# Optimization experiments

Measured on AMD Instinct MI355X. Metric: run time of the kernel, lower is better.

## Reference

```python
import jax, jax.numpy as jnp
import numpy as np

D = 1024          # n_embd
H = 4 * D         # SwiGLU hidden
E = 8             # num_experts
K = 2             # top_k
B, T = 2, 2048

def setup_inputs() -> dict:
    key = jax.random.key(0)
    ks = jax.random.split(key, 12)
    s = 0.02
    return {
        "x":   jax.random.normal(ks[0], (B, T, D), jnp.float32),
        "noise": jax.random.normal(ks[1], (B, T, E), jnp.float32),
        # router (nn.Linear with bias=True by default)
        "Wr": jax.random.normal(ks[2], (D, E), jnp.float32) * s,
        "br": jnp.zeros((E,), jnp.float32),
        "Wn": jax.random.normal(ks[3], (D, E), jnp.float32) * s,
        "bn": jnp.zeros((E,), jnp.float32),
        # routed experts, stacked over E (bias=False)
        "Wg": jax.random.normal(ks[4], (E, D, H), jnp.float32) * s,
        "Wu": jax.random.normal(ks[5], (E, D, H), jnp.float32) * s,
        "Wd": jax.random.normal(ks[6], (E, H, D), jnp.float32) * s,
        # shared expert (num_shared_experts = 1)
        "Sg": jax.random.normal(ks[7], (D, H), jnp.float32) * s,
        "Su": jax.random.normal(ks[8], (D, H), jnp.float32) * s,
        "Sd": jax.random.normal(ks[9], (H, D), jnp.float32) * s,
    }

def reference(x, noise, Wr, br, Wn, bn, Wg, Wu, Wd, Sg, Su, Sd):
    # shared expert: SwiGLU MLP over all tokens
    shared_out = (jax.nn.silu(x @ Sg) * (x @ Su)) @ Sd  # [B,T,D]

    # noisy top-k router
    logits = x @ Wr + br                                 # [B,T,E]
    noise_logits = x @ Wn + bn
    noisy = logits + noise * jax.nn.softplus(noise_logits)
    _, top_idx = jax.lax.top_k(noisy, K)                 # [B,T,K]
    sel = jax.nn.one_hot(top_idx, E, dtype=noisy.dtype).sum(-2) > 0  # [B,T,E]
    sparse = jnp.where(sel, noisy, -jnp.inf)
    gates = jax.nn.softmax(sparse, axis=-1)              # [B,T,E], 0 for unselected

    # original runs every expert densely over all tokens, weighted by gate
    g = jnp.einsum('btd,edh->beth', x, Wg)               # [B,E,T,H]
    u = jnp.einsum('btd,edh->beth', x, Wu)
    y = jnp.einsum('beth,ehd->betd', jax.nn.silu(g) * u, Wd)  # [B,E,T,D]
    routed = jnp.einsum('bte,betd->btd', gates, y)

    return shared_out + routed
```

## Files before the change

### kernel.cpp

```cpp
#include <hip/hip_runtime.h>

typedef unsigned short u16;
typedef unsigned int u32;
typedef __attribute__((ext_vector_type(8))) __bf16 bf16x8;
typedef __attribute__((ext_vector_type(4))) float f32x4;

#define D_ 1024
#define H_ 4096
#define E_ 8
#define NT_ 4096
#define RCAP_ 8448


__device__ __forceinline__ u16 f2b(float f) {
  u32 u = __float_as_uint(f);
  u += 0x7fffu + ((u >> 16) & 1u);
  return (u16)(u >> 16);
}

__device__ __forceinline__ void glds16(const u16* g, u16* l) {
  __builtin_amdgcn_global_load_lds((const __attribute__((address_space(1))) void*)g,
                                   (__attribute__((address_space(3))) void*)l, 16, 0, 0);
}

__global__ void init_ints(int* p, int n) {
  int i = threadIdx.x;
  if (i < n) p[i] = 0;
}

__global__ void pack_x(const float* __restrict__ x, u16* __restrict__ xp) {
  const int t = blockIdx.x, i = threadIdx.x;
  float4 v = ((const float4*)(x + (size_t)t * D_))[i];
  const int kb = i >> 4, ch = (i >> 1) & 7, sub = (i & 1) * 4;
  u16 tmp[4] = {f2b(v.x), f2b(v.y), f2b(v.z), f2b(v.w)};
  *(uint2*)(xp + ((size_t)kb * NT_ + t) * 64 + ((ch ^ (t & 7)) << 3) + sub) = *(uint2*)tmp;
}

__global__ void pack_b(const float* __restrict__ src, const float* __restrict__ src2,
                       u16* __restrict__ dst, int Kdim, int Rdim) {
  const int r0 = blockIdx.x * 64, k0 = blockIdx.y * 64, z = blockIdx.z;
  const int Rout = src2 ? (Rdim * 2) : Rdim;
  src += (size_t)z * Kdim * Rdim;
  if (src2) src2 += (size_t)z * Kdim * Rdim;
  u16* dkb = dst + (size_t)z * (Kdim >> 6) * Rout * 64 + (size_t)(k0 >> 6) * Rout * 64;
  __shared__ float t1[64][65];
  __shared__ float t2[64][65];
  const int tx = threadIdx.x, ty = threadIdx.y;
#pragma unroll
  for (int i = 0; i < 16; ++i) {
    const int kk = ty + 4 * i;
    t1[kk][tx] = src[(size_t)(k0 + kk) * Rdim + r0 + tx];
    if (src2) t2[kk][tx] = src2[(size_t)(k0 + kk) * Rdim + r0 + tx];
  }
  __syncthreads();
#pragma unroll
  for (int i = 0; i < 16; ++i) {
    const int rr = ty + 4 * i, r = r0 + rr;
    if (src2) {
      const int rg = 32 * (r >> 4) + (r & 15), ru = rg + 16;
      dkb[(size_t)rg * 64 + ((((tx >> 3) ^ (rg & 7)) << 3) | (tx & 7))] = f2b(t1[tx][rr]);
      dkb[(size_t)ru * 64 + ((((tx >> 3) ^ (ru & 7)) << 3) | (tx & 7))] = f2b(t2[tx][rr]);
    } else {
      dkb[(size_t)r * 64 + ((((tx >> 3) ^ (r & 7)) << 3) | (tx & 7))] = f2b(t1[tx][rr]);
    }
  }
}

__global__ void router_k(const float* __restrict__ x, const float* __restrict__ noise,
                         const float* __restrict__ Wr, const float* __restrict__ br,
                         const float* __restrict__ Wn, const float* __restrict__ bn,
                         int* __restrict__ counts, int* __restrict__ tok_e,
                         float* __restrict__ tok_g) {
  const int t = blockIdx.x;
  const int lane = threadIdx.x;
  float xv[16];
#pragma unroll
  for (int i = 0; i < 16; ++i) xv[i] = x[(size_t)t * D_ + lane + 64 * i];
  float nz[E_];
#pragma unroll
  for (int e = 0; e < E_; ++e) {
    float ar = 0.f, an = 0.f;
#pragma unroll
    for (int i = 0; i < 16; ++i) {
      int d = lane + 64 * i;
      ar += xv[i] * Wr[d * E_ + e];
      an += xv[i] * Wn[d * E_ + e];
    }
#pragma unroll
    for (int o = 32; o > 0; o >>= 1) {
      ar += __shfl_down(ar, o, 64);
      an += __shfl_down(an, o, 64);
    }
    if (lane == 0) {
      float lg = ar + br[e], nl = an + bn[e];
      float sp = (nl > 20.f) ? nl : log1pf(expf(nl));
      nz[e] = lg + noise[(size_t)t * E_ + e] * sp;
    }
  }
  if (lane == 0) {
    int i0 = 0;
#pragma unroll
    for (int e = 1; e < E_; ++e) if (nz[e] > nz[i0]) i0 = e;
    int i1 = (i0 == 0) ? 1 : 0;
#pragma unroll
    for (int e = 0; e < E_; ++e) if (e != i0 && nz[e] > nz[i1]) i1 = e;
    float a = nz[i0], b = nz[i1];
    float m = fmaxf(a, b);
    float ea = expf(a - m), eb = expf(b - m);
    float inv = 1.f / (ea + eb);
    tok_e[2 * t] = i0; tok_e[2 * t + 1] = i1;
    tok_g[2 * t] = ea * inv; tok_g[2 * t + 1] = eb * inv;
    atomicAdd(&counts[i0], 1);
    atomicAdd(&counts[i1], 1);
  }
}

__global__ void scan_k(const int* __restrict__ counts, int* __restrict__ offsets) {
  if (threadIdx.x == 0) {
    int acc = 0;
    for (int e = 0; e < E_; ++e) { offsets[e] = acc; acc += (counts[e] + 7) & ~7; }
    offsets[E_] = acc;
  }
}

__global__ void gather_k(const u16* __restrict__ xp, const int* __restrict__ tok_e,
                         const float* __restrict__ tok_g, const int* __restrict__ offsets,
                         int* __restrict__ cursors, u16* __restrict__ Xallp,
                         int* __restrict__ row_token, float* __restrict__ row_gate) {
  const int t = blockIdx.x;
  __shared__ int rws[2];
  if (threadIdx.x < 2) {
    int e = tok_e[2 * t + threadIdx.x];
    int r = offsets[e] + atomicAdd(&cursors[e], 1);
    row_token[r] = t;
    row_gate[r] = tok_g[2 * t + threadIdx.x];
    rws[threadIdx.x] = r;
  }
  __syncthreads();
  const int r0 = rws[0], r1 = rws[1];
  const int x7 = t & 7;
#pragma unroll
  for (int it = 0; it < 2; ++it) {
    const int u = threadIdx.x + 64 * it;
    const int kb = u >> 3, cs = u & 7;
    uint4 v = *(const uint4*)(xp + ((size_t)kb * NT_ + t) * 64 + (cs << 3));
    const int c = cs ^ x7;
    *(uint4*)(Xallp + ((size_t)kb * RCAP_ + r0) * 64 + ((c ^ (r0 & 7)) << 3)) = v;
    *(uint4*)(Xallp + ((size_t)kb * RCAP_ + r1) * 64 + ((c ^ (r1 & 7)) << 3)) = v;
  }
}

__device__ __forceinline__ void stage_tile(const u16* ga, const u16* gb,
                                           u16* la, u16* lb, int wv, int lane) {
#pragma unroll
  for (int c = 0; c < 4; ++c) {
    glds16(ga + (wv * 4 + c) * 512 + lane * 8, la + (wv * 4 + c) * 512);
    glds16(gb + (wv * 4 + c) * 512 + lane * 8, lb + (wv * 4 + c) * 512);
  }
}

__global__ __launch_bounds__(256, 2)
void gemm1_k(const u16* __restrict__ Ap, const u16* __restrict__ Bp, u16* __restrict__ actp,
             const int* __restrict__ neArr, const int* __restrict__ offArr,
             int fixedM, int K, int aRowCap) {
  int bx, by, e;
  if (neArr) {
    const int lid = blockIdx.x + 32 * (blockIdx.y + (int)gridDim.y * blockIdx.z);
    e = lid & 7; const int rest = lid >> 3; bx = rest & 31; by = rest >> 5;
  } else { bx = blockIdx.x; by = blockIdx.y; e = 0; }
  const int ne = neArr ? neArr[e] : fixedM;
  const int m0 = bx * 128;
  if (m0 >= ne) return;
  const int off = offArr ? offArr[e] : 0;
  const int NKB = K >> 6;
  const size_t aKS = (size_t)aRowCap * 64;
  const size_t bKS = (size_t)8192 * 64;
  const u16* A = Ap + (size_t)(off + m0) * 64;
  const u16* B = Bp + ((size_t)e * NKB * 8192 + (size_t)by * 128) * 64;

  __shared__ __align__(16) u16 As[2][128 * 64], Bs[2][128 * 64];

  const int tid = threadIdx.x, lane = tid & 63, wv = tid >> 6;
  const int wm = (wv >> 1) * 64, wn = (wv & 1) * 64;
  const int lm = lane & 15, lq = lane >> 4;
  const int c0 = ((lq ^ (lm & 7)) << 4);

  f32x4 acc[4][4] = {};

  stage_tile(A, B, As[0], Bs[0], wv, lane);
  stage_tile(A + aKS, B + bKS, As[1], Bs[1], wv, lane);
  asm volatile("s_waitcnt vmcnt(8)" ::: "memory");
  __builtin_amdgcn_s_barrier();
  __builtin_amdgcn_sched_barrier(0);

  for (int t = 0; t < NKB; ++t) {
    const u16* as = As[t & 1];
    const u16* bs = Bs[t & 1];
#pragma unroll
    for (int ks = 0; ks < 2; ++ks) {
      const int kc = c0 ^ (ks << 6);
      bf16x8 af[4], bb[4];
#pragma unroll
      for (int i = 0; i < 4; ++i) {
        af[i] = *(const bf16x8*)((const char*)as + (wm + i * 16 + lm) * 128 + kc);
        bb[i] = *(const bf16x8*)((const char*)bs + (wn + i * 16 + lm) * 128 + kc);
      }
#pragma unroll
      for (int i = 0; i < 4; ++i)
#pragma unroll
        for (int j = 0; j < 4; ++j)
          acc[i][j] = __builtin_amdgcn_mfma_f32_16x16x32_bf16(af[i], bb[j], acc[i][j], 0, 0, 0);
    }
    if (t + 1 < NKB) {
      __builtin_amdgcn_s_barrier();
      __builtin_amdgcn_sched_barrier(0);
      if (t + 2 < NKB) {
        stage_tile(A + (size_t)(t + 2) * aKS, B + (size_t)(t + 2) * bKS,
                   As[t & 1], Bs[t & 1], wv, lane);
        asm volatile("s_waitcnt vmcnt(8)" ::: "memory");
      } else {
        asm volatile("s_waitcnt vmcnt(0)" ::: "memory");
      }
      __builtin_amdgcn_sched_barrier(0);
      __builtin_amdgcn_s_barrier();
      __builtin_amdgcn_sched_barrier(0);
    }
  }

  const int hbase = (wn >> 1);
#pragma unroll
  for (int i = 0; i < 4; ++i)
#pragma unroll
    for (int r = 0; r < 4; ++r) {
      const int m = m0 + wm + i * 16 + lq * 4 + r;
      if (m < ne) {
        const int row = off + m;
        u16* dr = actp + ((size_t)by * RCAP_ + row) * 64;
        const int r7 = row & 7;
#pragma unroll
        for (int jj = 0; jj < 2; ++jj) {
          float g = acc[i][2 * jj][r], u = acc[i][2 * jj + 1][r];
          float s = g / (1.f + __expf(-g)) * u;
          const int hl = hbase + jj * 16 + lm;
          dr[(((hl >> 3) ^ r7) << 3) | (hl & 7)] = f2b(s);
        }
      }
    }
}

__global__ __launch_bounds__(256, 2)
void gemm2_k(const u16* __restrict__ Ap, const u16* __restrict__ Bp,
             float* __restrict__ out,
             const int* __restrict__ neArr, const int* __restrict__ offArr,
             const int* __restrict__ row_token, const float* __restrict__ row_gate,
             int fixedM, int K) {
  int bx, by, e;
  if (neArr) {
    const int lid = blockIdx.x + 32 * (blockIdx.y + (int)gridDim.y * blockIdx.z);
    e = lid & 7; const int rest = lid >> 3; bx = rest & 31; by = rest >> 5;
  } else { bx = blockIdx.x; by = blockIdx.y; e = 0; }
  const int ne = neArr ? neArr[e] : fixedM;
  const int m0 = bx * 128;
  if (m0 >= ne) return;
  const int off = offArr ? offArr[e] : 0;
  const int NKB = K >> 6;
  const size_t aKS = (size_t)RCAP_ * 64;
  const size_t bKS = (size_t)1024 * 64;
  const u16* A = Ap + (size_t)(off + m0) * 64;
  const u16* B = Bp + ((size_t)e * NKB * 1024 + (size_t)by * 128) * 64;

  __shared__ __align__(16) u16 As[2][128 * 64], Bs[2][128 * 64];

  const int tid = threadIdx.x, lane = tid & 63, wv = tid >> 6;
  const int wm = (wv >> 1) * 64, wn = (wv & 1) * 64;
  const int lm = lane & 15, lq = lane >> 4;
  const int c0 = ((lq ^ (lm & 7)) << 4);

  f32x4 acc[4][4] = {};

  stage_tile(A, B, As[0], Bs[0], wv, lane);
  stage_tile(A + aKS, B + bKS, As[1], Bs[1], wv, lane);
  asm volatile("s_waitcnt vmcnt(8)" ::: "memory");
  __builtin_amdgcn_s_barrier();
  __builtin_amdgcn_sched_barrier(0);

  for (int t = 0; t < NKB; ++t) {
    const u16* as = As[t & 1];
    const u16* bs = Bs[t & 1];
#pragma unroll
    for (int ks = 0; ks < 2; ++ks) {
      const int kc = c0 ^ (ks << 6);
      bf16x8 af[4], bb[4];
#pragma unroll
      for (int i = 0; i < 4; ++i) {
        af[i] = *(const bf16x8*)((const char*)as + (wm + i * 16 + lm) * 128 + kc);
        bb[i] = *(const bf16x8*)((const char*)bs + (wn + i * 16 + lm) * 128 + kc);
      }
#pragma unroll
      for (int i = 0; i < 4; ++i)
#pragma unroll
        for (int j = 0; j < 4; ++j)
          acc[i][j] = __builtin_amdgcn_mfma_f32_16x16x32_bf16(af[i], bb[j], acc[i][j], 0, 0, 0);
    }
    if (t + 1 < NKB) {
      __builtin_amdgcn_s_barrier();
      __builtin_amdgcn_sched_barrier(0);
      if (t + 2 < NKB) {
        stage_tile(A + (size_t)(t + 2) * aKS, B + (size_t)(t + 2) * bKS,
                   As[t & 1], Bs[t & 1], wv, lane);
        asm volatile("s_waitcnt vmcnt(8)" ::: "memory");
      } else {
        asm volatile("s_waitcnt vmcnt(0)" ::: "memory");
      }
      __builtin_amdgcn_sched_barrier(0);
      __builtin_amdgcn_s_barrier();
      __builtin_amdgcn_sched_barrier(0);
    }
  }

#pragma unroll
  for (int i = 0; i < 4; ++i)
#pragma unroll
    for (int r = 0; r < 4; ++r) {
      const int m = m0 + wm + i * 16 + lq * 4 + r;
      if (m < ne) {
        const int n = by * 128 + wn + lm;
        if (row_token) {
          const int t = row_token[off + m];
          const float gt = row_gate[off + m];
#pragma unroll
          for (int j = 0; j < 4; ++j)
            atomicAdd(out + (size_t)t * D_ + n + j * 16, gt * acc[i][j][r]);
        } else {
#pragma unroll
          for (int j = 0; j < 4; ++j)
            out[(size_t)m * D_ + n + j * 16] = acc[i][j][r];
        }
      }
    }
}

extern "C" void kernel_launch(void* const* d_in, const int* in_sizes, int n_in,
                              void* d_out, int out_size, void* d_ws, size_t ws_size,
                              hipStream_t stream) {
  const float* x     = (const float*)d_in[0];
  const float* noise = (const float*)d_in[1];
  const float* Wr    = (const float*)d_in[2];
  const float* br    = (const float*)d_in[3];
  const float* Wn    = (const float*)d_in[4];
  const float* bn    = (const float*)d_in[5];
  const float* Wg    = (const float*)d_in[6];
  const float* Wu    = (const float*)d_in[7];
  const float* Wd    = (const float*)d_in[8];
  const float* Sg    = (const float*)d_in[9];
  const float* Su    = (const float*)d_in[10];
  const float* Sd    = (const float*)d_in[11];
  float* out = (float*)d_out;

  char* base = (char*)d_ws;
  size_t off = 0;
  auto take = [&](size_t bytes) -> void* {
    void* r = base + off;
    off = (off + bytes + 255) & ~(size_t)255;
    return r;
  };
  u16* Wgup = (u16*)take((size_t)E_ * 16 * 8192 * 64 * 2);
  u16* Wdp  = (u16*)take((size_t)E_ * 64 * 1024 * 64 * 2);
  u16* Sgup = (u16*)take((size_t)16 * 8192 * 64 * 2);
  u16* Sdp  = (u16*)take((size_t)64 * 1024 * 64 * 2);
  u16* xp   = (u16*)take((size_t)16 * NT_ * 64 * 2);
  u16* Xallp = (u16*)take((size_t)16 * RCAP_ * 64 * 2);
  u16* actp  = (u16*)take((size_t)64 * RCAP_ * 64 * 2);
  int*   row_token = (int*)take(RCAP_ * 4);
  float* row_gate  = (float*)take(RCAP_ * 4);
  int*   tok_e = (int*)take(NT_ * 2 * 4);
  float* tok_g = (float*)take(NT_ * 2 * 4);
  int* ints = (int*)take(32 * 4);
  int* counts = ints, *cursors = ints + 8, *offsets = ints + 16;
  if (off > ws_size) return;

  hipLaunchKernelGGL(init_ints, dim3(1), dim3(64), 0, stream, ints, 32);
  hipLaunchKernelGGL(pack_x, dim3(NT_), dim3(256), 0, stream, x, xp);
  dim3 tb(64, 4);
  hipLaunchKernelGGL(pack_b, dim3(H_ / 64, D_ / 64, E_), tb, 0, stream, Wg, Wu, Wgup, D_, H_);
  hipLaunchKernelGGL(pack_b, dim3(D_ / 64, H_ / 64, E_), tb, 0, stream,
                     Wd, (const float*)nullptr, Wdp, H_, D_);
  hipLaunchKernelGGL(pack_b, dim3(H_ / 64, D_ / 64, 1), tb, 0, stream, Sg, Su, Sgup, D_, H_);
  hipLaunchKernelGGL(pack_b, dim3(D_ / 64, H_ / 64, 1), tb, 0, stream,
                     Sd, (const float*)nullptr, Sdp, H_, D_);

  hipLaunchKernelGGL(router_k, dim3(NT_), dim3(64), 0, stream,
                     x, noise, Wr, br, Wn, bn, counts, tok_e, tok_g);
  hipLaunchKernelGGL(scan_k, dim3(1), dim3(64), 0, stream, counts, offsets);
  hipLaunchKernelGGL(gather_k, dim3(NT_), dim3(64), 0, stream,
                     xp, tok_e, tok_g, offsets, cursors, Xallp, row_token, row_gate);

  hipLaunchKernelGGL(gemm1_k, dim3(32, 64, 1), dim3(256), 0, stream,
                     xp, Sgup, actp, (const int*)nullptr, (const int*)nullptr, NT_, D_, NT_);
  hipLaunchKernelGGL(gemm2_k, dim3(32, 8, 1), dim3(256), 0, stream,
                     actp, Sdp, out, (const int*)nullptr, (const int*)nullptr,
                     (const int*)nullptr, (const float*)nullptr, NT_, H_);
  hipLaunchKernelGGL(gemm1_k, dim3(32, 64, E_), dim3(256), 0, stream,
                     Xallp, Wgup, actp, counts, offsets, 0, D_, RCAP_);
  hipLaunchKernelGGL(gemm2_k, dim3(32, 8, E_), dim3(256), 0, stream,
                     actp, Wdp, out, counts, offsets, row_token, row_gate, 0, H_);
}
```

Before: 1.577 ms.

## Use 256x256 GEMM tiles with 8 waves and interleaved half-tile prefetch

Replaces the 128x128, 4-wave GEMM core with a shared 256x256, 8-wave core. Each wave computes 128x64 and loads the next K-block's A and B in half-tile chunks, interleaved between MFMA groups, with s_setprio raised around the MFMAs. The larger tile is meant to raise arithmetic intensity and cut global and LDS traffic per FLOP, and the interleaving is meant to hide load latency. The pack_b kernel now writes 16-byte vectors instead of scalar u16 stores, and RCAP grows to pad for 256-row tiles. In exchange it uses more registers and LDS per block, launches fewer blocks, and wastes more work on partially filled expert tiles.

```diff
diff --git a/kernel.cpp b/kernel.cpp
--- a/kernel.cpp
+++ b/kernel.cpp
@@ -9,7 +9,10 @@
 #define H_ 4096
 #define E_ 8
 #define NT_ 4096
-#define RCAP_ 8448
+#define RCAP_ 8704
+
+#define LDSH_ 8192
+#define LDST_ 16384
 
 
 __device__ __forceinline__ u16 f2b(float f) {
@@ -21,6 +24,12 @@
 __device__ __forceinline__ void glds16(const u16* g, u16* l) {
   __builtin_amdgcn_global_load_lds((const __attribute__((address_space(1))) void*)g,
                                    (__attribute__((address_space(3))) void*)l, 16, 0, 0);
+}
+
+__device__ __forceinline__ void stage_half(const u16* __restrict__ g, u16* l, int wv, int lane) {
+#pragma unroll
+  for (int c = 0; c < 2; ++c)
+    glds16(g + c * 4096 + wv * 512 + lane * 8, l + c * 4096 + wv * 512);
 }
 
 __global__ void init_ints(int* p, int n) {
@@ -53,15 +62,28 @@
     if (src2) t2[kk][tx] = src2[(size_t)(k0 + kk) * Rdim + r0 + tx];
   }
   __syncthreads();
-#pragma unroll
-  for (int i = 0; i < 16; ++i) {
-    const int rr = ty + 4 * i, r = r0 + rr;
+  const int idx = ty * 64 + tx;
+  const int ch = idx & 7, rl0 = idx >> 3;
+#pragma unroll
+  for (int half = 0; half < 2; ++half) {
+    const int rl = rl0 + 32 * half;
+    const int r = r0 + rl;
     if (src2) {
       const int rg = 32 * (r >> 4) + (r & 15), ru = rg + 16;
-      dkb[(size_t)rg * 64 + ((((tx >> 3) ^ (rg & 7)) << 3) | (tx & 7))] = f2b(t1[tx][rr]);
-      dkb[(size_t)ru * 64 + ((((tx >> 3) ^ (ru & 7)) << 3) | (tx & 7))] = f2b(t2[tx][rr]);
+      const int kg = (ch ^ (rg & 7)) << 3;
+      union { u16 v[8]; uint4 q; } pg, pu;
+#pragma unroll
+      for (int j = 0; j < 8; ++j) pg.v[j] = f2b(t1[kg + j][rl]);
+#pragma unroll
+      for (int j = 0; j < 8; ++j) pu.v[j] = f2b(t2[kg + j][rl]);
+      *(uint4*)(dkb + (size_t)rg * 64 + ch * 8) = pg.q;
+      *(uint4*)(dkb + (size_t)ru * 64 + ch * 8) = pu.q;
     } else {
-      dkb[(size_t)r * 64 + ((((tx >> 3) ^ (r & 7)) << 3) | (tx & 7))] = f2b(t1[tx][rr]);
+      const int kc = (ch ^ (r & 7)) << 3;
+      union { u16 v[8]; uint4 q; } pk;
+#pragma unroll
+      for (int j = 0; j < 8; ++j) pk.v[j] = f2b(t1[kc + j][rl]);
+      *(uint4*)(dkb + (size_t)r * 64 + ch * 8) = pk.q;
     }
   }
 }
@@ -150,105 +172,145 @@
   }
 }
 
-__device__ __forceinline__ void stage_tile(const u16* ga, const u16* gb,
-                                           u16* la, u16* lb, int wv, int lane) {
-#pragma unroll
-  for (int c = 0; c < 4; ++c) {
-    glds16(ga + (wv * 4 + c) * 512 + lane * 8, la + (wv * 4 + c) * 512);
-    glds16(gb + (wv * 4 + c) * 512 + lane * 8, lb + (wv * 4 + c) * 512);
-  }
-}
-
-__global__ __launch_bounds__(256, 2)
+__device__ __forceinline__ void gemm_core8(
+    const u16* __restrict__ A, const u16* __restrict__ B,
+    size_t aKS, size_t bKS, int NKB,
+    u16* As, u16* Bs, f32x4 acc[8][4], int tid) {
+  const int lane = tid & 63, wv = tid >> 6;
+  const int wr = wv >> 2, wc = wv & 3;
+  const int lm = lane & 15, lq = lane >> 4;
+  const int c0 = ((lq ^ (lm & 7)) << 4);
+  const char* asr = (const char*)As + (wr * 128 + lm) * 128;
+  const char* bsr = (const char*)Bs + (wc * 64 + lm) * 128;
+
+  stage_half(A,         As,         wv, lane);
+  stage_half(A + LDSH_, As + LDSH_, wv, lane);
+  stage_half(B,         Bs,         wv, lane);
+  stage_half(B + LDSH_, Bs + LDSH_, wv, lane);
+  stage_half(A + aKS,   As + LDST_, wv, lane);
+  asm volatile("s_waitcnt vmcnt(2)" ::: "memory");
+  __builtin_amdgcn_s_barrier();
+  __builtin_amdgcn_sched_barrier(0);
+
+  for (int t = 0; t < NKB; ++t) {
+    const int bo = (t & 1) << 15;
+    const int ou = ((t & 1) ^ 1) * LDST_;
+    bf16x8 a[8], bb[4];
+#pragma unroll
+    for (int i = 0; i < 8; ++i)
+      a[i] = *(const bf16x8*)(asr + bo + i * 2048 + c0);
+#pragma unroll
+    for (int j = 0; j < 4; ++j)
+      bb[j] = *(const bf16x8*)(bsr + bo + j * 2048 + c0);
+    if (t + 1 < NKB) stage_half(A + (size_t)(t + 1) * aKS + LDSH_, As + ou + LDSH_, wv, lane);
+    asm volatile("s_waitcnt lgkmcnt(8)" ::: "memory");
+    __builtin_amdgcn_s_barrier();
+    asm volatile("s_waitcnt lgkmcnt(0)" ::: "memory");
+    __builtin_amdgcn_sched_barrier(0);
+    __builtin_amdgcn_s_setprio(1);
+#pragma unroll
+    for (int i = 0; i < 4; ++i)
+#pragma unroll
+      for (int j = 0; j < 4; ++j)
+        acc[i][j] = __builtin_amdgcn_mfma_f32_16x16x32_bf16(a[i], bb[j], acc[i][j], 0, 0, 0);
+    __builtin_amdgcn_s_setprio(0);
+    __builtin_amdgcn_s_barrier();
+    if (t + 1 < NKB) stage_half(B + (size_t)(t + 1) * bKS, Bs + ou, wv, lane);
+    __builtin_amdgcn_s_barrier();
+    __builtin_amdgcn_sched_barrier(0);
+    __builtin_amdgcn_s_setprio(1);
+#pragma unroll
+    for (int i = 0; i < 4; ++i)
+#pragma unroll
+      for (int j = 0; j < 4; ++j)
+        acc[4 + i][j] = __builtin_amdgcn_mfma_f32_16x16x32_bf16(a[4 + i], bb[j], acc[4 + i][j], 0, 0, 0);
+    __builtin_amdgcn_s_setprio(0);
+    __builtin_amdgcn_s_barrier();
+#pragma unroll
+    for (int i = 0; i < 8; ++i)
+      a[i] = *(const bf16x8*)(asr + bo + i * 2048 + (c0 ^ 64));
+#pragma unroll
+    for (int j = 0; j < 4; ++j)
+      bb[j] = *(const bf16x8*)(bsr + bo + j * 2048 + (c0 ^ 64));
+    if (t + 1 < NKB) stage_half(B + (size_t)(t + 1) * bKS + LDSH_, Bs + ou + LDSH_, wv, lane);
+    asm volatile("s_waitcnt lgkmcnt(8)" ::: "memory");
+    __builtin_amdgcn_s_barrier();
+    asm volatile("s_waitcnt lgkmcnt(0)" ::: "memory");
+    __builtin_amdgcn_sched_barrier(0);
+    __builtin_amdgcn_s_setprio(1);
+#pragma unroll
+    for (int i = 0; i < 4; ++i)
+#pragma unroll
+      for (int j = 0; j < 4; ++j)
+        acc[i][j] = __builtin_amdgcn_mfma_f32_16x16x32_bf16(a[i], bb[j], acc[i][j], 0, 0, 0);
+    __builtin_amdgcn_s_setprio(0);
+    __builtin_amdgcn_s_barrier();
+    if (t + 2 < NKB) stage_half(A + (size_t)(t + 2) * aKS, As + (bo >> 1), wv, lane);
+    __builtin_amdgcn_s_barrier();
+    __builtin_amdgcn_sched_barrier(0);
+    __builtin_amdgcn_s_setprio(1);
+#pragma unroll
+    for (int i = 0; i < 4; ++i)
+#pragma unroll
+      for (int j = 0; j < 4; ++j)
+        acc[4 + i][j] = __builtin_amdgcn_mfma_f32_16x16x32_bf16(a[4 + i], bb[j], acc[4 + i][j], 0, 0, 0);
+    __builtin_amdgcn_s_setprio(0);
+    if (t + 1 < NKB) {
+      if (t + 2 < NKB) { asm volatile("s_waitcnt vmcnt(2)" ::: "memory"); }
+      else             { asm volatile("s_waitcnt vmcnt(0)" ::: "memory"); }
+      __builtin_amdgcn_sched_barrier(0);
+      __builtin_amdgcn_s_barrier();
+    }
+  }
+}
+
+__global__ __launch_bounds__(512, 2)
 void gemm1_k(const u16* __restrict__ Ap, const u16* __restrict__ Bp, u16* __restrict__ actp,
              const int* __restrict__ neArr, const int* __restrict__ offArr,
              int fixedM, int K, int aRowCap) {
   int bx, by, e;
   if (neArr) {
-    const int lid = blockIdx.x + 32 * (blockIdx.y + (int)gridDim.y * blockIdx.z);
-    e = lid & 7; const int rest = lid >> 3; bx = rest & 31; by = rest >> 5;
+    const int lid = blockIdx.x + (int)gridDim.x * (blockIdx.y + (int)gridDim.y * blockIdx.z);
+    e = lid & 7; const int rest = lid >> 3; bx = rest & 15; by = rest >> 4;
   } else { bx = blockIdx.x; by = blockIdx.y; e = 0; }
   const int ne = neArr ? neArr[e] : fixedM;
-  const int m0 = bx * 128;
+  const int m0 = bx * 256;
   if (m0 >= ne) return;
   const int off = offArr ? offArr[e] : 0;
+  const int n0 = by * 256;
   const int NKB = K >> 6;
-  const size_t aKS = (size_t)aRowCap * 64;
-  const size_t bKS = (size_t)8192 * 64;
   const u16* A = Ap + (size_t)(off + m0) * 64;
-  const u16* B = Bp + ((size_t)e * NKB * 8192 + (size_t)by * 128) * 64;
-
-  __shared__ __align__(16) u16 As[2][128 * 64], Bs[2][128 * 64];
-
-  const int tid = threadIdx.x, lane = tid & 63, wv = tid >> 6;
-  const int wm = (wv >> 1) * 64, wn = (wv & 1) * 64;
+  const u16* B = Bp + ((size_t)e * NKB * 8192 + (size_t)n0) * 64;
+
+  __shared__ __align__(16) u16 As[2 * LDST_], Bs[2 * LDST_];
+  f32x4 acc[8][4] = {};
+  const int tid = threadIdx.x;
+  gemm_core8(A, B, (size_t)aRowCap * 64, (size_t)8192 * 64, NKB, As, Bs, acc, tid);
+
+  const int lane = tid & 63, wv = tid >> 6;
+  const int wr = wv >> 2, wc = wv & 3;
   const int lm = lane & 15, lq = lane >> 4;
-  const int c0 = ((lq ^ (lm & 7)) << 4);
-
-  f32x4 acc[4][4] = {};
-
-  stage_tile(A, B, As[0], Bs[0], wv, lane);
-  stage_tile(A + aKS, B + bKS, As[1], Bs[1], wv, lane);
-  asm volatile("s_waitcnt vmcnt(8)" ::: "memory");
-  __builtin_amdgcn_s_barrier();
-  __builtin_amdgcn_sched_barrier(0);
-
-  for (int t = 0; t < NKB; ++t) {
-    const u16* as = As[t & 1];
-    const u16* bs = Bs[t & 1];
-#pragma unroll
-    for (int ks = 0; ks < 2; ++ks) {
-      const int kc = c0 ^ (ks << 6);
-      bf16x8 af[4], bb[4];
-#pragma unroll
-      for (int i = 0; i < 4; ++i) {
-        af[i] = *(const bf16x8*)((const char*)as + (wm + i * 16 + lm) * 128 + kc);
-        bb[i] = *(const bf16x8*)((const char*)bs + (wn + i * 16 + lm) * 128 + kc);
-      }
-#pragma unroll
-      for (int i = 0; i < 4; ++i)
-#pragma unroll
-        for (int j = 0; j < 4; ++j)
-          acc[i][j] = __builtin_amdgcn_mfma_f32_16x16x32_bf16(af[i], bb[j], acc[i][j], 0, 0, 0);
-    }
-    if (t + 1 < NKB) {
-      __builtin_amdgcn_s_barrier();
-      __builtin_amdgcn_sched_barrier(0);
-      if (t + 2 < NKB) {
-        stage_tile(A + (size_t)(t + 2) * aKS, B + (size_t)(t + 2) * bKS,
-                   As[t & 1], Bs[t & 1], wv, lane);
-        asm volatile("s_waitcnt vmcnt(8)" ::: "memory");
-      } else {
-        asm volatile("s_waitcnt vmcnt(0)" ::: "memory");
-      }
-      __builtin_amdgcn_sched_barrier(0);
-      __builtin_amdgcn_s_barrier();
-      __builtin_amdgcn_sched_barrier(0);
-    }
-  }
-
-  const int hbase = (wn >> 1);
-#pragma unroll
-  for (int i = 0; i < 4; ++i)
+  const int hb = (n0 + wc * 64) >> 1;
+#pragma unroll
+  for (int i = 0; i < 8; ++i)
 #pragma unroll
     for (int r = 0; r < 4; ++r) {
-      const int m = m0 + wm + i * 16 + lq * 4 + r;
+      const int m = m0 + wr * 128 + i * 16 + lq * 4 + r;
       if (m < ne) {
         const int row = off + m;
-        u16* dr = actp + ((size_t)by * RCAP_ + row) * 64;
         const int r7 = row & 7;
 #pragma unroll
         for (int jj = 0; jj < 2; ++jj) {
           float g = acc[i][2 * jj][r], u = acc[i][2 * jj + 1][r];
           float s = g / (1.f + __expf(-g)) * u;
-          const int hl = hbase + jj * 16 + lm;
-          dr[(((hl >> 3) ^ r7) << 3) | (hl & 7)] = f2b(s);
+          const int h = hb + jj * 16 + lm;
+          actp[((size_t)(h >> 6) * RCAP_ + row) * 64 + ((((h >> 3) & 7) ^ r7) << 3 | (h & 7))] = f2b(s);
         }
       }
     }
 }
 
-__global__ __launch_bounds__(256, 2)
+__global__ __launch_bounds__(512, 2)
 void gemm2_k(const u16* __restrict__ Ap, const u16* __restrict__ Bp,
              float* __restrict__ out,
              const int* __restrict__ neArr, const int* __restrict__ offArr,
@@ -256,81 +318,39 @@
              int fixedM, int K) {
   int bx, by, e;
   if (neArr) {
-    const int lid = blockIdx.x + 32 * (blockIdx.y + (int)gridDim.y * blockIdx.z);
-    e = lid & 7; const int rest = lid >> 3; bx = rest & 31; by = rest >> 5;
+    const int lid = blockIdx.x + (int)gridDim.x * (blockIdx.y + (int)gridDim.y * blockIdx.z);
+    e = lid & 7; const int rest = lid >> 3; bx = rest & 15; by = rest >> 4;
   } else { bx = blockIdx.x; by = blockIdx.y; e = 0; }
   const int ne = neArr ? neArr[e] : fixedM;
-  const int m0 = bx * 128;
+  const int m0 = bx * 256;
   if (m0 >= ne) return;
   const int off = offArr ? offArr[e] : 0;
+  const int n0 = by * 256;
   const int NKB = K >> 6;
-  const size_t aKS = (size_t)RCAP_ * 64;
-  const size_t bKS = (size_t)1024 * 64;
   const u16* A = Ap + (size_t)(off + m0) * 64;
-  const u16* B = Bp + ((size_t)e * NKB * 1024 + (size_t)by * 128) * 64;
-
-  __shared__ __align__(16) u16 As[2][128 * 64], Bs[2][128 * 64];
-
-  const int tid = threadIdx.x, lane = tid & 63, wv = tid >> 6;
-  const int wm = (wv >> 1) * 64, wn = (wv & 1) * 64;
+  const u16* B = Bp + ((size_t)e * NKB * 1024 + (size_t)n0) * 64;
+
+  __shared__ __align__(16) u16 As[2 * LDST_], Bs[2 * LDST_];
+  f32x4 acc[8][4] = {};
+  const int tid = threadIdx.x;
+  gemm_core8(A, B, (size_t)RCAP_ * 64, (size_t)1024 * 64, NKB, As, Bs, acc, tid);
+
+  const int lane = tid & 63, wv = tid >> 6;
+  const int wr = wv >> 2, wc = wv & 3;
   const int lm = lane & 15, lq = lane >> 4;
-  const int c0 = ((lq ^ (lm & 7)) << 4);
-
-  f32x4 acc[4][4] = {};
-
-  stage_tile(A, B, As[0], Bs[0], wv, lane);
-  stage_tile(A + aKS, B + bKS, As[1], Bs[1], wv, lane);
-  asm volatile("s_waitcnt vmcnt(8)" ::: "memory");
-  __builtin_amdgcn_s_barrier();
-  __builtin_amdgcn_sched_barrier(0);
-
-  for (int t = 0; t < NKB; ++t) {
-    const u16* as = As[t & 1];
-    const u16* bs = Bs[t & 1];
-#pragma unroll
-    for (int ks = 0; ks < 2; ++ks) {
-      const int kc = c0 ^ (ks << 6);
-      bf16x8 af[4], bb[4];
-#pragma unroll
-      for (int i = 0; i < 4; ++i) {
-        af[i] = *(const bf16x8*)((const char*)as + (wm + i * 16 + lm) * 128 + kc);
-        bb[i] = *(const bf16x8*)((const char*)bs + (wn + i * 16 + lm) * 128 + kc);
-      }
-#pragma unroll
-      for (int i = 0; i < 4; ++i)
-#pragma unroll
-        for (int j = 0; j < 4; ++j)
-          acc[i][j] = __builtin_amdgcn_mfma_f32_16x16x32_bf16(af[i], bb[j], acc[i][j], 0, 0, 0);
-    }
-    if (t + 1 < NKB) {
-      __builtin_amdgcn_s_barrier();
-      __builtin_amdgcn_sched_barrier(0);
-      if (t + 2 < NKB) {
-        stage_tile(A + (size_t)(t + 2) * aKS, B + (size_t)(t + 2) * bKS,
-                   As[t & 1], Bs[t & 1], wv, lane);
-        asm volatile("s_waitcnt vmcnt(8)" ::: "memory");
-      } else {
-        asm volatile("s_waitcnt vmcnt(0)" ::: "memory");
-      }
-      __builtin_amdgcn_sched_barrier(0);
-      __builtin_amdgcn_s_barrier();
-      __builtin_amdgcn_sched_barrier(0);
-    }
-  }
-
-#pragma unroll
-  for (int i = 0; i < 4; ++i)
+#pragma unroll
+  for (int i = 0; i < 8; ++i)
 #pragma unroll
     for (int r = 0; r < 4; ++r) {
-      const int m = m0 + wm + i * 16 + lq * 4 + r;
+      const int m = m0 + wr * 128 + i * 16 + lq * 4 + r;
       if (m < ne) {
-        const int n = by * 128 + wn + lm;
+        const int n = n0 + wc * 64 + lm;
         if (row_token) {
-          const int t = row_token[off + m];
+          const int tkn = row_token[off + m];
           const float gt = row_gate[off + m];
 #pragma unroll
           for (int j = 0; j < 4; ++j)
-            atomicAdd(out + (size_t)t * D_ + n + j * 16, gt * acc[i][j][r]);
+            atomicAdd(out + (size_t)tkn * D_ + n + j * 16, gt * acc[i][j][r]);
         } else {
 #pragma unroll
           for (int j = 0; j < 4; ++j)
@@ -395,13 +415,13 @@
   hipLaunchKernelGGL(gather_k, dim3(NT_), dim3(64), 0, stream,
                      xp, tok_e, tok_g, offsets, cursors, Xallp, row_token, row_gate);
 
-  hipLaunchKernelGGL(gemm1_k, dim3(32, 64, 1), dim3(256), 0, stream,
+  hipLaunchKernelGGL(gemm1_k, dim3(16, 32, 1), dim3(512), 0, stream,
                      xp, Sgup, actp, (const int*)nullptr, (const int*)nullptr, NT_, D_, NT_);
-  hipLaunchKernelGGL(gemm2_k, dim3(32, 8, 1), dim3(256), 0, stream,
+  hipLaunchKernelGGL(gemm2_k, dim3(16, 4, 1), dim3(512), 0, stream,
                      actp, Sdp, out, (const int*)nullptr, (const int*)nullptr,
                      (const int*)nullptr, (const float*)nullptr, NT_, H_);
-  hipLaunchKernelGGL(gemm1_k, dim3(32, 64, E_), dim3(256), 0, stream,
+  hipLaunchKernelGGL(gemm1_k, dim3(16, 32, E_), dim3(512), 0, stream,
                      Xallp, Wgup, actp, counts, offsets, 0, D_, RCAP_);
-  hipLaunchKernelGGL(gemm2_k, dim3(32, 8, E_), dim3(256), 0, stream,
+  hipLaunchKernelGGL(gemm2_k, dim3(16, 4, E_), dim3(512), 0, stream,
                      actp, Wdp, out, counts, offsets, row_token, row_gate, 0, H_);
 }
```

After: 1.537 ms. 1.03x faster.
